# Performance work log

Measured on AMD Instinct MI355X. Metric: run time of the kernel, lower is better.

## Reference

```python
import jax, jax.numpy as jnp
import numpy as np

V = 50257   # vocab_size
H = 1024    # hidden_size + 8
L = 2048    # input_length
ML = 2048   # max_length


def setup_inputs() -> dict:
    key = jax.random.key(0)
    ks = jax.random.split(key, 12)
    def w(k, shape, scale=0.02):
        return jax.random.normal(k, shape, dtype=jnp.float32) * scale
    return {
        'decoder_input': jax.random.randint(ks[0], (1, 1), 0, V),
        'hidden_state': jax.random.normal(ks[1], (1, 1, H), dtype=jnp.float32),
        'encoder_outputs': jax.random.normal(ks[2], (ML, H), dtype=jnp.float32),
        'input_variable': jax.random.randint(ks[3], (L, 1), 0, V),
        'embedding': w(ks[4], (V, H), 1.0),
        'W_attn_w': w(ks[5], (ML, 2 * H)), 'b_attn_w': jnp.zeros((ML,), jnp.float32),
        'W_attn_u': w(ks[6], (H, 2 * H)), 'b_attn_u': jnp.zeros((H,), jnp.float32),
        'W_ih': w(ks[7], (3 * H, H)), 'b_ih': jnp.zeros((3 * H,), jnp.float32),
        'W_hh': w(ks[8], (3 * H, H)), 'b_hh': jnp.zeros((3 * H,), jnp.float32),
        'W_copy': w(ks[9], (H, H)), 'b_copy': jnp.zeros((H,), jnp.float32),
        'W_gen': w(ks[10], (V, H)), 'b_gen': jnp.zeros((V,), jnp.float32),
    }


def _forward(decoder_input, hidden_state, encoder_outputs, input_variable,
             embedding, W_attn_w, b_attn_w, W_attn_u, b_attn_u,
             W_ih, b_ih, W_hh, b_hh, W_copy, b_copy, W_gen, b_gen):
    # batch_size = 1, single decode step (dropout is identity at inference)
    emb0 = embedding[decoder_input].reshape(1, H)           # (1, H)
    h0 = hidden_state[0]                                    # (1, H) previous hidden

    # attention over encoder outputs
    cat_eh = jnp.concatenate([emb0, h0], axis=1)            # (1, 2H)
    attn_weights = jax.nn.softmax(cat_eh @ W_attn_w.T + b_attn_w, axis=1)  # (1, ML)
    attn_applied = attn_weights @ encoder_outputs           # (1, H)

    joined = jnp.concatenate([emb0, attn_applied], axis=1)  # (1, 2H)
    rnn_in = jax.nn.relu(joined @ W_attn_u.T + b_attn_u)    # (1, H)

    # one GRU step (PyTorch gate layout: r, z, n)
    gi = rnn_in @ W_ih.T + b_ih                             # (1, 3H)
    gh = h0 @ W_hh.T + b_hh                                 # (1, 3H)
    r = jax.nn.sigmoid(gi[:, :H] + gh[:, :H])
    z = jax.nn.sigmoid(gi[:, H:2 * H] + gh[:, H:2 * H])
    n = jnp.tanh(gi[:, 2 * H:] + r * gh[:, 2 * H:])
    h_new = (1.0 - z) * n + z * h0                          # (1, H)
    final_hidden = h_new[None]                              # (1, 1, H)

    # generate + copy scores
    score_g = h_new @ W_gen.T + b_gen                       # (1, V)
    trimmed = encoder_outputs[:L]                           # (L, H)
    score_c = jnp.tanh(trimmed @ W_copy.T + b_copy) @ h0[0] # (L,)  bmm with OLD hidden
    probs = jax.nn.softmax(jnp.concatenate([score_g, score_c[None]], axis=1), axis=1)
    prob_g = probs[:, :V]                                   # (1, V)
    prob_c = probs[:, V:]                                   # (1, L)

    # copy->vocab: scatter-add (math-equivalent to dense one-hot bmm)
    idx = input_variable[:, 0]                              # (L,) int
    prob_c_to_g = jnp.zeros((V,), probs.dtype).at[idx].add(prob_c[0])[None]
    final_output = prob_g + prob_c_to_g                     # (1, V)

    # selective read: attend only to positions matching the current input token
    din = decoder_input[0, 0]
    matched = (idx == din).astype(probs.dtype)              # (L,)
    final_weights = ((prob_c * matched) @ trimmed)[:, None, :]  # (1, 1, H)
    return final_output, final_hidden, final_weights


def reference(decoder_input, hidden_state, encoder_outputs, input_variable,
              embedding, W_attn_w, b_attn_w, W_attn_u, b_attn_u,
              W_ih, b_ih, W_hh, b_hh, W_copy, b_copy, W_gen, b_gen):
    return _forward(decoder_input, hidden_state, encoder_outputs, input_variable,
                    embedding, W_attn_w, b_attn_w, W_attn_u, b_attn_u,
                    W_ih, b_ih, W_hh, b_hh, W_copy, b_copy, W_gen, b_gen)
```

## Files before the change

### kernel.cpp

```cpp
#include <hip/hip_runtime.h>
#include <math.h>

#define VSZ 50257
#define HSZ 1024
#define LSZ 2048
#define SHIFT 60.0f

__global__ void k_attn(const float* __restrict__ Waw, const float* __restrict__ baw,
                       const int* __restrict__ din, const float* __restrict__ emb,
                       const float* __restrict__ h0, float* __restrict__ attnw,
                       float* __restrict__ out, float* __restrict__ score_c,
                       float* __restrict__ acc, float* __restrict__ psum) {
  int bid = blockIdx.x, tid = threadIdx.x;
  if (bid < 512) {
    int gw = bid * 4 + (tid >> 6);
    int lane = tid & 63;
    const float4* row = (const float4*)(Waw + (size_t)gw * 2048);
    const float4* e4 = (const float4*)(emb + (size_t)din[0] * HSZ);
    const float4* h4 = (const float4*)h0;
    float s = 0.f;
#pragma unroll
    for (int j = 0; j < 4; ++j) {
      float4 a = row[lane + 64 * j];
      float4 b = e4[lane + 64 * j];
      s += a.x * b.x + a.y * b.y + a.z * b.z + a.w * b.w;
    }
#pragma unroll
    for (int j = 0; j < 4; ++j) {
      float4 a = row[256 + lane + 64 * j];
      float4 b = h4[lane + 64 * j];
      s += a.x * b.x + a.y * b.y + a.z * b.z + a.w * b.w;
    }
#pragma unroll
    for (int o = 32; o > 0; o >>= 1) s += __shfl_down(s, o, 64);
    if (lane == 0) attnw[gw] = s + baw[gw];
  } else if (bid < 709) {
    int v = (bid - 512) * 256 + tid;
    if (v < VSZ) out[v] = 0.f;
  } else if (bid == 709) {
#pragma unroll
    for (int k = 0; k < 8; ++k) score_c[tid + 256 * k] = 0.f;
  } else {
#pragma unroll
    for (int k = 0; k < 4; ++k) acc[tid + 256 * k] = 0.f;
    if (tid == 0) psum[0] = 0.f;
  }
}

__global__ void k_attn_apply(const float* __restrict__ attnw, const float* __restrict__ enc,
                             float* __restrict__ acc) {
  __shared__ float red[256];
  __shared__ float sw[64];
  int bid = blockIdx.x, t = threadIdx.x;
  int hb = bid & 3, mb = bid >> 2;
  float m = -1e30f;
  for (int i = t; i < LSZ; i += 256) m = fmaxf(m, attnw[i]);
  red[t] = m; __syncthreads();
  for (int s = 128; s > 0; s >>= 1) { if (t < s) red[t] = fmaxf(red[t], red[t + s]); __syncthreads(); }
  float gmax = red[0]; __syncthreads();
  float sum = 0.f;
  for (int i = t; i < LSZ; i += 256) sum += expf(attnw[i] - gmax);
  red[t] = sum; __syncthreads();
  for (int s = 128; s > 0; s >>= 1) { if (t < s) red[t] += red[t + s]; __syncthreads(); }
  float inv = 1.f / red[0];
  if (t < 64) sw[t] = expf(attnw[mb * 64 + t] - gmax) * inv;
  __syncthreads();
  int h = hb * 256 + t;
  float s = 0.f;
#pragma unroll 4
  for (int j = 0; j < 64; ++j) s = fmaf(sw[j], enc[(size_t)(mb * 64 + j) * HSZ + h], s);
  atomicAdd(&acc[h], s);
}

__global__ void k_rnn(const float* __restrict__ Wau, const float* __restrict__ bau,
                      const int* __restrict__ din, const float* __restrict__ emb,
                      const float* __restrict__ acc, float* __restrict__ rnn_in) {
  int gw = blockIdx.x * 4 + (threadIdx.x >> 6);
  int lane = threadIdx.x & 63;
  const float4* row = (const float4*)(Wau + (size_t)gw * 2048);
  const float4* e4 = (const float4*)(emb + (size_t)din[0] * HSZ);
  const float4* a4 = (const float4*)acc;
  float s = 0.f;
#pragma unroll
  for (int j = 0; j < 4; ++j) {
    float4 a = row[lane + 64 * j];
    float4 b = e4[lane + 64 * j];
    s += a.x * b.x + a.y * b.y + a.z * b.z + a.w * b.w;
  }
#pragma unroll
  for (int j = 0; j < 4; ++j) {
    float4 a = row[256 + lane + 64 * j];
    float4 b = a4[lane + 64 * j];
    s += a.x * b.x + a.y * b.y + a.z * b.z + a.w * b.w;
  }
#pragma unroll
  for (int o = 32; o > 0; o >>= 1) s += __shfl_down(s, o, 64);
  if (lane == 0) rnn_in[gw] = fmaxf(s + bau[gw], 0.f);
}

__global__ void k_gates(const float* __restrict__ Wih, const float* __restrict__ bih,
                        const float* __restrict__ xin, const float* __restrict__ Whh,
                        const float* __restrict__ bhh, const float* __restrict__ h0,
                        float* __restrict__ y) {
  int gw = blockIdx.x * 4 + (threadIdx.x >> 6);
  int lane = threadIdx.x & 63;
  const float* W; const float* x; float bv; int r;
  if (gw < 3 * HSZ) { W = Wih; x = xin; r = gw; bv = bih[r]; }
  else              { W = Whh; x = h0;  r = gw - 3 * HSZ; bv = bhh[r]; }
  const float4* row = (const float4*)(W + (size_t)r * HSZ);
  const float4* xv = (const float4*)x;
  float s = 0.f;
#pragma unroll
  for (int j = 0; j < 4; ++j) {
    float4 a = row[lane + 64 * j];
    float4 b = xv[lane + 64 * j];
    s += a.x * b.x + a.y * b.y + a.z * b.z + a.w * b.w;
  }
#pragma unroll
  for (int o = 32; o > 0; o >>= 1) s += __shfl_down(s, o, 64);
  if (lane == 0) y[gw] = s + bv;
}

__global__ void k_gru(const float* __restrict__ gi, const float* __restrict__ gh,
                      const float* __restrict__ h0, float* __restrict__ h_new,
                      float* __restrict__ out) {
  int t = blockIdx.x * 256 + threadIdx.x;
  float r = 1.f / (1.f + expf(-(gi[t] + gh[t])));
  float z = 1.f / (1.f + expf(-(gi[HSZ + t] + gh[HSZ + t])));
  float n = tanhf(gi[2 * HSZ + t] + r * gh[2 * HSZ + t]);
  float hn = (1.f - z) * n + z * h0[t];
  h_new[t] = hn;
  out[VSZ + t] = hn;
  out[VSZ + HSZ + t] = 0.f;
}

__global__ __launch_bounds__(256) void k_big(
    const float* __restrict__ enc, const float* __restrict__ Wc,
    const float* __restrict__ bc, const float* __restrict__ hvec,
    const float* __restrict__ Wg, const float* __restrict__ bg,
    const float* __restrict__ h_new, float* __restrict__ score) {
  __shared__ float As[32][128];
  __shared__ float Bs[32][64];
  int bid = blockIdx.x, tid = threadIdx.x;
  if (bid < 256) {
    int lt = bid & 15, ht = bid >> 4;
    int tx = tid & 15, ty = tid >> 4;
    const int l0 = lt * 128, h0r = ht * 64;
    float acc[8][4] = {};
    for (int kb = 0; kb < HSZ; kb += 32) {
      __syncthreads();
#pragma unroll
      for (int i = 0; i < 4; ++i) {
        int fi = tid + 256 * i;
        int l = fi >> 3, kq = fi & 7;
        float4 v = *(const float4*)&enc[(size_t)(l0 + l) * HSZ + kb + kq * 4];
        As[kq * 4 + 0][l] = v.x; As[kq * 4 + 1][l] = v.y;
        As[kq * 4 + 2][l] = v.z; As[kq * 4 + 3][l] = v.w;
      }
#pragma unroll
      for (int i = 0; i < 2; ++i) {
        int fi = tid + 256 * i;
        int h = fi >> 3, kq = fi & 7;
        float4 v = *(const float4*)&Wc[(size_t)(h0r + h) * HSZ + kb + kq * 4];
        Bs[kq * 4 + 0][h] = v.x; Bs[kq * 4 + 1][h] = v.y;
        Bs[kq * 4 + 2][h] = v.z; Bs[kq * 4 + 3][h] = v.w;
      }
      __syncthreads();
#pragma unroll
      for (int k = 0; k < 32; ++k) {
        float4 b4 = *(const float4*)&Bs[k][tx * 4];
        float4 a0 = *(const float4*)&As[k][ty * 8];
        float4 a1 = *(const float4*)&As[k][ty * 8 + 4];
        float av[8] = {a0.x, a0.y, a0.z, a0.w, a1.x, a1.y, a1.z, a1.w};
        float bv[4] = {b4.x, b4.y, b4.z, b4.w};
#pragma unroll
        for (int i = 0; i < 8; ++i)
#pragma unroll
          for (int j = 0; j < 4; ++j) acc[i][j] = fmaf(av[i], bv[j], acc[i][j]);
      }
    }
    float hw[4], bcv[4];
#pragma unroll
    for (int j = 0; j < 4; ++j) {
      int h = h0r + tx * 4 + j;
      bcv[j] = bc[h];
      hw[j] = hvec[h];
    }
    __syncthreads();
    float (*rs)[17] = (float (*)[17])&As[0][0];
#pragma unroll
    for (int i = 0; i < 8; ++i) {
      float p = 0.f;
#pragma unroll
      for (int j = 0; j < 4; ++j) p += tanhf(acc[i][j] + bcv[j]) * hw[j];
      rs[ty * 8 + i][tx] = p;
    }
    __syncthreads();
    if (tid < 128) {
      float s = 0.f;
#pragma unroll
      for (int x = 0; x < 16; ++x) s += rs[tid][x];
      atomicAdd(&score[VSZ + l0 + tid], s);
    }
  } else {
    int gw = (bid - 256) * 4 + (tid >> 6);
    int lane = tid & 63;
    if (gw >= VSZ) return;
    const float4* row = (const float4*)(Wg + (size_t)gw * HSZ);
    const float4* xv = (const float4*)h_new;
    float s = 0.f;
#pragma unroll
    for (int j = 0; j < 4; ++j) {
      float4 a = row[lane + 64 * j];
      float4 b = xv[lane + 64 * j];
      s += a.x * b.x + a.y * b.y + a.z * b.z + a.w * b.w;
    }
#pragma unroll
    for (int o = 32; o > 0; o >>= 1) s += __shfl_down(s, o, 64);
    if (lane == 0) score[gw] = s + bg[gw];
  }
}

__global__ void k_sum(const float* __restrict__ score, float* __restrict__ psum) {
  __shared__ float sh[256];
  int t = threadIdx.x, b = blockIdx.x;
  float s = 0.f;
  for (int i = b * 256 + t; i < VSZ + LSZ; i += 64 * 256) s += expf(score[i] - SHIFT);
  sh[t] = s; __syncthreads();
  for (int s2 = 128; s2 > 0; s2 >>= 1) { if (t < s2) sh[t] += sh[t + s2]; __syncthreads(); }
  if (t == 0) atomicAdd(psum, sh[0]);
}

__global__ void k_final(const float* __restrict__ score, const float* __restrict__ psum,
                        const int* __restrict__ idx, const int* __restrict__ din,
                        const float* __restrict__ enc, float* __restrict__ out) {
  int bid = blockIdx.x, t = threadIdx.x;
  float inv = 1.f / psum[0];
  if (bid < 197) {
    int v = bid * 256 + t;
    if (v < VSZ) atomicAdd(&out[v], expf(score[v] - SHIFT) * inv);
  } else {
    __shared__ float pm[256];
    __shared__ int flag;
    if (t == 0) flag = 0;
    __syncthreads();
    int l0 = (bid - 197) * 256;
    int l = l0 + t;
    float p = expf(score[VSZ + l] - SHIFT) * inv;
    atomicAdd(&out[idx[l]], p);
    int matched = (idx[l] == din[0]);
    pm[t] = matched ? p : 0.f;
    if (matched) atomicExch(&flag, 1);
    __syncthreads();
    if (flag) {
      for (int h = t; h < HSZ; h += 256) {
        float s = 0.f;
        for (int l2 = 0; l2 < 256; ++l2)
          if (pm[l2] != 0.f) s = fmaf(pm[l2], enc[(size_t)(l0 + l2) * HSZ + h], s);
        if (s != 0.f) atomicAdd(&out[VSZ + HSZ + h], s);
      }
    }
  }
}

extern "C" void kernel_launch(void* const* d_in, const int* in_sizes, int n_in,
                              void* d_out, int out_size, void* d_ws, size_t ws_size,
                              hipStream_t stream) {
  const int*   din = (const int*)d_in[0];
  const float* h0  = (const float*)d_in[1];
  const float* enc = (const float*)d_in[2];
  const int*   idx = (const int*)d_in[3];
  const float* emb = (const float*)d_in[4];
  const float* Waw = (const float*)d_in[5];
  const float* baw = (const float*)d_in[6];
  const float* Wau = (const float*)d_in[7];
  const float* bau = (const float*)d_in[8];
  const float* Wih = (const float*)d_in[9];
  const float* bih = (const float*)d_in[10];
  const float* Whh = (const float*)d_in[11];
  const float* bhh = (const float*)d_in[12];
  const float* Wc  = (const float*)d_in[13];
  const float* bc  = (const float*)d_in[14];
  const float* Wg  = (const float*)d_in[15];
  const float* bg  = (const float*)d_in[16];
  float* out = (float*)d_out;
  float* ws  = (float*)d_ws;

  float* acc    = ws;
  float* rnn_in = ws + 1024;
  float* gi     = ws + 2048;
  float* gh     = ws + 5120;
  float* h_new  = ws + 8192;
  float* attnw  = ws + 9216;
  float* score  = ws + 11264;
  float* psum   = ws + 63576;

  k_attn<<<711, 256, 0, stream>>>(Waw, baw, din, emb, h0, attnw, out, score + VSZ, acc, psum);
  k_attn_apply<<<128, 256, 0, stream>>>(attnw, enc, acc);
  k_rnn<<<256, 256, 0, stream>>>(Wau, bau, din, emb, acc, rnn_in);
  k_gates<<<1536, 256, 0, stream>>>(Wih, bih, rnn_in, Whh, bhh, h0, gi);
  k_gru<<<4, 256, 0, stream>>>(gi, gh, h0, h_new, out);
  k_big<<<256 + (VSZ + 3) / 4, 256, 0, stream>>>(enc, Wc, bc, h0, Wg, bg, h_new, score);
  k_sum<<<64, 256, 0, stream>>>(score, psum);
  k_final<<<205, 256, 0, stream>>>(score, psum, idx, din, enc, out);
}
```

Baseline: 516.0 us.

## Use bf16 MFMA for copy-score GEMM and two rows per wave for vocab GEMV

The encoder and W_copy matrices are converted to bf16 in extra blocks of the first kernel. The copy-score GEMM then runs on MFMA 16x16x32 bf16 instructions that load operands directly from global memory, with no LDS tiling. The vocab GEMV now handles two rows per wave so each load of h_new is reused. The change adds a conversion pass of about 12 MB of reads and 6 MB of writes, and it lowers the copy-score precision to bf16.

```diff
diff --git a/kernel.cpp b/kernel.cpp
--- a/kernel.cpp
+++ b/kernel.cpp
@@ -6,11 +6,22 @@
 #define LSZ 2048
 #define SHIFT 60.0f
 
+typedef __attribute__((ext_vector_type(8))) short bf16x8;
+typedef __attribute__((ext_vector_type(4))) float f32x4;
+
+__device__ __forceinline__ unsigned short f2bf(float f) {
+  unsigned int u = __float_as_uint(f);
+  u += 0x7FFFu + ((u >> 16) & 1u);
+  return (unsigned short)(u >> 16);
+}
+
 __global__ void k_attn(const float* __restrict__ Waw, const float* __restrict__ baw,
                        const int* __restrict__ din, const float* __restrict__ emb,
-                       const float* __restrict__ h0, float* __restrict__ attnw,
+                       const float* __restrict__ h0, const float* __restrict__ enc,
+                       const float* __restrict__ Wc, float* __restrict__ attnw,
                        float* __restrict__ out, float* __restrict__ score_c,
-                       float* __restrict__ acc, float* __restrict__ psum) {
+                       float* __restrict__ acc, float* __restrict__ psum,
+                       unsigned short* __restrict__ bfbuf) {
   int bid = blockIdx.x, tid = threadIdx.x;
   if (bid < 512) {
     int gw = bid * 4 + (tid >> 6);
@@ -40,10 +51,22 @@
   } else if (bid == 709) {
 #pragma unroll
     for (int k = 0; k < 8; ++k) score_c[tid + 256 * k] = 0.f;
-  } else {
+  } else if (bid == 710) {
 #pragma unroll
     for (int k = 0; k < 4; ++k) acc[tid + 256 * k] = 0.f;
     if (tid == 0) psum[0] = 0.f;
+  } else {
+    int cb = bid - 711;
+#pragma unroll
+    for (int c = 0; c < 4; ++c) {
+      int g = cb * 1024 + c * 256 + tid;
+      float4 v;
+      if (g < 524288) v = ((const float4*)enc)[g];
+      else            v = ((const float4*)Wc)[g - 524288];
+      ushort4 o;
+      o.x = f2bf(v.x); o.y = f2bf(v.y); o.z = f2bf(v.z); o.w = f2bf(v.w);
+      *(ushort4*)(bfbuf + (size_t)g * 4) = o;
+    }
   }
 }
 
@@ -134,90 +157,73 @@
   out[VSZ + HSZ + t] = 0.f;
 }
 
-__global__ __launch_bounds__(256) void k_big(
-    const float* __restrict__ enc, const float* __restrict__ Wc,
+__global__ __launch_bounds__(256) void k_huge(
+    const unsigned short* __restrict__ encB, const unsigned short* __restrict__ WcB,
     const float* __restrict__ bc, const float* __restrict__ hvec,
     const float* __restrict__ Wg, const float* __restrict__ bg,
     const float* __restrict__ h_new, float* __restrict__ score) {
-  __shared__ float As[32][128];
-  __shared__ float Bs[32][64];
   int bid = blockIdx.x, tid = threadIdx.x;
-  if (bid < 256) {
-    int lt = bid & 15, ht = bid >> 4;
-    int tx = tid & 15, ty = tid >> 4;
-    const int l0 = lt * 128, h0r = ht * 64;
-    float acc[8][4] = {};
-    for (int kb = 0; kb < HSZ; kb += 32) {
-      __syncthreads();
-#pragma unroll
-      for (int i = 0; i < 4; ++i) {
-        int fi = tid + 256 * i;
-        int l = fi >> 3, kq = fi & 7;
-        float4 v = *(const float4*)&enc[(size_t)(l0 + l) * HSZ + kb + kq * 4];
-        As[kq * 4 + 0][l] = v.x; As[kq * 4 + 1][l] = v.y;
-        As[kq * 4 + 2][l] = v.z; As[kq * 4 + 3][l] = v.w;
+  int wave = tid >> 6, lane = tid & 63;
+  if (bid < 512) {
+    int l0 = (bid >> 4) * 64 + wave * 16;
+    int h0r = (bid & 15) * 64;
+    int col = lane & 15, quad = lane >> 4;
+    f32x4 acc[4] = {};
+    const unsigned short* arow = encB + ((size_t)(l0 + col) << 10) + quad * 8;
+#pragma unroll 4
+    for (int k0 = 0; k0 < HSZ; k0 += 32) {
+      bf16x8 a = *(const bf16x8*)(arow + k0);
+#pragma unroll
+      for (int ht = 0; ht < 4; ++ht) {
+        bf16x8 b = *(const bf16x8*)(WcB + ((size_t)(h0r + ht * 16 + col) << 10) + k0 + quad * 8);
+        acc[ht] = __builtin_amdgcn_mfma_f32_16x16x32_bf16(a, b, acc[ht], 0, 0, 0);
       }
-#pragma unroll
-      for (int i = 0; i < 2; ++i) {
-        int fi = tid + 256 * i;
-        int h = fi >> 3, kq = fi & 7;
-        float4 v = *(const float4*)&Wc[(size_t)(h0r + h) * HSZ + kb + kq * 4];
-        Bs[kq * 4 + 0][h] = v.x; Bs[kq * 4 + 1][h] = v.y;
-        Bs[kq * 4 + 2][h] = v.z; Bs[kq * 4 + 3][h] = v.w;
-      }
-      __syncthreads();
-#pragma unroll
-      for (int k = 0; k < 32; ++k) {
-        float4 b4 = *(const float4*)&Bs[k][tx * 4];
-        float4 a0 = *(const float4*)&As[k][ty * 8];
-        float4 a1 = *(const float4*)&As[k][ty * 8 + 4];
-        float av[8] = {a0.x, a0.y, a0.z, a0.w, a1.x, a1.y, a1.z, a1.w};
-        float bv[4] = {b4.x, b4.y, b4.z, b4.w};
-#pragma unroll
-        for (int i = 0; i < 8; ++i)
-#pragma unroll
-          for (int j = 0; j < 4; ++j) acc[i][j] = fmaf(av[i], bv[j], acc[i][j]);
-      }
-    }
-    float hw[4], bcv[4];
-#pragma unroll
-    for (int j = 0; j < 4; ++j) {
-      int h = h0r + tx * 4 + j;
-      bcv[j] = bc[h];
-      hw[j] = hvec[h];
-    }
-    __syncthreads();
-    float (*rs)[17] = (float (*)[17])&As[0][0];
-#pragma unroll
-    for (int i = 0; i < 8; ++i) {
-      float p = 0.f;
-#pragma unroll
-      for (int j = 0; j < 4; ++j) p += tanhf(acc[i][j] + bcv[j]) * hw[j];
-      rs[ty * 8 + i][tx] = p;
-    }
-    __syncthreads();
-    if (tid < 128) {
-      float s = 0.f;
-#pragma unroll
-      for (int x = 0; x < 16; ++x) s += rs[tid][x];
-      atomicAdd(&score[VSZ + l0 + tid], s);
+    }
+    float rsum[4] = {0.f, 0.f, 0.f, 0.f};
+#pragma unroll
+    for (int ht = 0; ht < 4; ++ht) {
+      int h = h0r + ht * 16 + col;
+      float bch = bc[h], hw = hvec[h];
+#pragma unroll
+      for (int r = 0; r < 4; ++r) rsum[r] += tanhf(acc[ht][r] + bch) * hw;
+    }
+#pragma unroll
+    for (int o = 1; o < 16; o <<= 1) {
+#pragma unroll
+      for (int r = 0; r < 4; ++r) rsum[r] += __shfl_xor(rsum[r], o, 64);
+    }
+    if (col == 0) {
+      int lrow = l0 + quad * 4;
+#pragma unroll
+      for (int r = 0; r < 4; ++r) atomicAdd(&score[VSZ + lrow + r], rsum[r]);
     }
   } else {
-    int gw = (bid - 256) * 4 + (tid >> 6);
-    int lane = tid & 63;
-    if (gw >= VSZ) return;
-    const float4* row = (const float4*)(Wg + (size_t)gw * HSZ);
+    int r0 = (bid - 512) * 8 + wave * 2;
+    int ra = r0 < VSZ ? r0 : VSZ - 1;
+    int rb = r0 + 1 < VSZ ? r0 + 1 : VSZ - 1;
     const float4* xv = (const float4*)h_new;
-    float s = 0.f;
-#pragma unroll
-    for (int j = 0; j < 4; ++j) {
-      float4 a = row[lane + 64 * j];
-      float4 b = xv[lane + 64 * j];
-      s += a.x * b.x + a.y * b.y + a.z * b.z + a.w * b.w;
-    }
-#pragma unroll
-    for (int o = 32; o > 0; o >>= 1) s += __shfl_down(s, o, 64);
-    if (lane == 0) score[gw] = s + bg[gw];
+    float4 x0 = xv[lane], x1 = xv[lane + 64], x2 = xv[lane + 128], x3 = xv[lane + 192];
+    const float4* p0 = (const float4*)(Wg + (size_t)ra * HSZ);
+    const float4* p1 = (const float4*)(Wg + (size_t)rb * HSZ);
+    float4 a0 = p0[lane], a1 = p0[lane + 64], a2 = p0[lane + 128], a3 = p0[lane + 192];
+    float4 b0 = p1[lane], b1 = p1[lane + 64], b2 = p1[lane + 128], b3 = p1[lane + 192];
+    float s0 = a0.x * x0.x + a0.y * x0.y + a0.z * x0.z + a0.w * x0.w
+             + a1.x * x1.x + a1.y * x1.y + a1.z * x1.z + a1.w * x1.w
+             + a2.x * x2.x + a2.y * x2.y + a2.z * x2.z + a2.w * x2.w
+             + a3.x * x3.x + a3.y * x3.y + a3.z * x3.z + a3.w * x3.w;
+    float s1 = b0.x * x0.x + b0.y * x0.y + b0.z * x0.z + b0.w * x0.w
+             + b1.x * x1.x + b1.y * x1.y + b1.z * x1.z + b1.w * x1.w
+             + b2.x * x2.x + b2.y * x2.y + b2.z * x2.z + b2.w * x2.w
+             + b3.x * x3.x + b3.y * x3.y + b3.z * x3.z + b3.w * x3.w;
+#pragma unroll
+    for (int o = 32; o > 0; o >>= 1) {
+      s0 += __shfl_down(s0, o, 64);
+      s1 += __shfl_down(s1, o, 64);
+    }
+    if (lane == 0) {
+      if (r0 < VSZ) score[r0] = s0 + bg[r0];
+      if (r0 + 1 < VSZ) score[r0 + 1] = s1 + bg[r0 + 1];
+    }
   }
 }
 
@@ -289,18 +295,21 @@
   float* acc    = ws;
   float* rnn_in = ws + 1024;
   float* gi     = ws + 2048;
-  float* gh     = ws + 5120;
   float* h_new  = ws + 8192;
   float* attnw  = ws + 9216;
   float* score  = ws + 11264;
-  float* psum   = ws + 63576;
-
-  k_attn<<<711, 256, 0, stream>>>(Waw, baw, din, emb, h0, attnw, out, score + VSZ, acc, psum);
+  float* psum   = ws + 63616;
+  unsigned short* bfbuf = (unsigned short*)(ws + 64000);
+  unsigned short* encB = bfbuf;
+  unsigned short* WcB  = bfbuf + 2097152;
+
+  k_attn<<<1479, 256, 0, stream>>>(Waw, baw, din, emb, h0, enc, Wc, attnw, out,
+                                   score + VSZ, acc, psum, bfbuf);
   k_attn_apply<<<128, 256, 0, stream>>>(attnw, enc, acc);
   k_rnn<<<256, 256, 0, stream>>>(Wau, bau, din, emb, acc, rnn_in);
   k_gates<<<1536, 256, 0, stream>>>(Wih, bih, rnn_in, Whh, bhh, h0, gi);
-  k_gru<<<4, 256, 0, stream>>>(gi, gh, h0, h_new, out);
-  k_big<<<256 + (VSZ + 3) / 4, 256, 0, stream>>>(enc, Wc, bc, h0, Wg, bg, h_new, score);
+  k_gru<<<4, 256, 0, stream>>>(gi, gi + 3072, h0, h_new, out);
+  k_huge<<<512 + (VSZ + 7) / 8, 256, 0, stream>>>(encB, WcB, bc, h0, Wg, bg, h_new, score);
   k_sum<<<64, 256, 0, stream>>>(score, psum);
   k_final<<<205, 256, 0, stream>>>(score, psum, idx, din, enc, out);
 }
```

Measured after the change: 463.5 us. 10.2% less time.
